# Performance work log

Measured on AMD Instinct MI355X. Metric: run time of the kernel, lower is better.

The kernel has to match this reference:

```python
import jax, jax.numpy as jnp
import numpy as np

B, S, D = 2, 2048, 4096
H, HKV, HD = 32, 8, 128          # heads, kv heads, head_dim
G = H // HKV                      # query groups per kv head
THETA = 10000.0


def setup_inputs() -> dict:
    key = jax.random.key(0)
    ks = jax.random.split(key, 6)
    s = 0.02
    return {
        "hidden_states": jax.random.normal(ks[0], (B, S, D), jnp.float32),
        "position_ids": jnp.broadcast_to(jnp.arange(S, dtype=jnp.int32), (B, S)),
        "attention_mask": jnp.ones((B, S), jnp.int32),
        "Wq": jax.random.normal(ks[1], (D, H * HD), jnp.float32) * s,
        "Wk": jax.random.normal(ks[2], (D, HKV * HD), jnp.float32) * s,
        "Wv": jax.random.normal(ks[3], (D, HKV * HD), jnp.float32) * s,
        "Wo": jax.random.normal(ks[4], (H * HD, D), jnp.float32) * s,
    }


def _rope_neox(x, positions):
    # x: [B, S, h, HD]; neox style: rotate halves
    half = HD // 2
    inv_freq = 1.0 / (THETA ** (jnp.arange(0, half, dtype=jnp.float32) / half))
    freqs = positions.astype(jnp.float32)[..., None] * inv_freq  # [B,S,half]
    cos = jnp.cos(freqs)[:, :, None, :]
    sin = jnp.sin(freqs)[:, :, None, :]
    x1, x2 = x[..., :half], x[..., half:]
    return jnp.concatenate([x1 * cos - x2 * sin, x2 * cos + x1 * sin], axis=-1)


def reference(hidden_states, position_ids, attention_mask, Wq, Wk, Wv, Wo):
    q = (hidden_states @ Wq).reshape(B, S, H, HD)
    k = (hidden_states @ Wk).reshape(B, S, HKV, HD)
    v = (hidden_states @ Wv).reshape(B, S, HKV, HD)

    q = _rope_neox(q, position_ids)
    k = _rope_neox(k, position_ids)

    # GQA: group query heads onto kv heads
    qg = q.reshape(B, S, HKV, G, HD)
    scale = HD ** -0.5
    scores = jnp.einsum("bqhgd,bkhd->bhgqk", qg, k) * scale  # [B,HKV,G,S,S]

    causal = jnp.tril(jnp.ones((S, S), bool))
    mask = causal[None, None, None] & (attention_mask[:, None, None, None, :] > 0)
    scores = jnp.where(mask, scores, jnp.finfo(scores.dtype).min)
    probs = jax.nn.softmax(scores, axis=-1)

    ctx = jnp.einsum("bhgqk,bkhd->bqhgd", probs, v).reshape(B, S, H * HD)
    return ctx @ Wo
```

## Files before the change

### kernel.cpp

```cpp
#include <hip/hip_runtime.h>
#include <hip/hip_bf16.h>
#include <cstdint>
#include <cstddef>

#define BB 2
#define SS 2048
#define DD 4096
#define HH 32
#define HKV 8
#define HDIM 128
#define NQKV 6144

typedef __attribute__((ext_vector_type(8))) short bf16x8;
typedef __attribute__((ext_vector_type(4))) float f32x4;

#define GLOAD_LDS16(g, l) __builtin_amdgcn_global_load_lds( \
    (const __attribute__((address_space(1))) void*)(g), \
    (__attribute__((address_space(3))) void*)(l), 16, 0, 0)

__global__ void cast_bf16_kernel(const float* __restrict__ in,
                                 __hip_bfloat16* __restrict__ out, int n4) {
  int i = blockIdx.x * 256 + threadIdx.x;
  if (i >= n4) return;
  float4 v = ((const float4*)in)[i];
  union { __hip_bfloat16 h[4]; short4 s4; } u;
  u.h[0] = __float2bfloat16(v.x);
  u.h[1] = __float2bfloat16(v.y);
  u.h[2] = __float2bfloat16(v.z);
  u.h[3] = __float2bfloat16(v.w);
  ((short4*)out)[i] = u.s4;
}

__global__ void transpose_cast4_kernel(const float* __restrict__ Wq,
                                       const float* __restrict__ Wk,
                                       const float* __restrict__ Wv,
                                       const float* __restrict__ Wo,
                                       __hip_bfloat16* __restrict__ WqkvT,
                                       __hip_bfloat16* __restrict__ WoT) {
  __shared__ float tile[32][33];
  int id = blockIdx.x;
  const float* W; __hip_bfloat16* WT; int C, bx, by;
  if (id < 16384)      { W = Wq; WT = WqkvT;                         C = 4096; int l = id;         bx = l & 127; by = l >> 7; }
  else if (id < 20480) { W = Wk; WT = WqkvT + (size_t)4096 * 4096;   C = 1024; int l = id - 16384; bx = l & 31;  by = l >> 5; }
  else if (id < 24576) { W = Wv; WT = WqkvT + (size_t)5120 * 4096;   C = 1024; int l = id - 20480; bx = l & 31;  by = l >> 5; }
  else                 { W = Wo; WT = WoT;                           C = 4096; int l = id - 24576; bx = l & 127; by = l >> 7; }
  const int R = 4096;
  int c0 = bx * 32, r0 = by * 32;
  int tx = threadIdx.x, ty = threadIdx.y;
#pragma unroll
  for (int i = 0; i < 32; i += 8)
    tile[ty + i][tx] = W[(size_t)(r0 + ty + i) * C + c0 + tx];
  __syncthreads();
#pragma unroll
  for (int i = 0; i < 32; i += 8)
    WT[(size_t)(c0 + ty + i) * R + r0 + tx] = __float2bfloat16(tile[tx][ty + i]);
}

__global__ void vt_kernel(const __hip_bfloat16* __restrict__ QKV,
                          __hip_bfloat16* __restrict__ VT) {
  __shared__ __hip_bfloat16 tile[32][33];
  int c0 = blockIdx.x * 32;
  int r0 = blockIdx.y * 32;
  int tx = threadIdx.x, ty = threadIdx.y;
#pragma unroll
  for (int i = 0; i < 32; i += 8)
    tile[ty + i][tx] = QKV[(size_t)(r0 + ty + i) * NQKV + 5120 + c0 + tx];
  __syncthreads();
#pragma unroll
  for (int i = 0; i < 32; i += 8) {
    int r = r0 + tx;
    int c = c0 + ty + i;
    VT[((size_t)(r >> 11) * 1024 + c) * SS + (r & 2047)] = tile[tx][ty + i];
  }
}

__global__ void rope_kernel(__hip_bfloat16* __restrict__ QKV,
                            const int* __restrict__ pos_ids) {
  int r = blockIdx.x;
  float fpos = (float)pos_ids[r];
  __hip_bfloat16* row = QKV + (size_t)r * NQKV;
  for (int p = threadIdx.x; p < 2560; p += 256) {
    int base, i;
    if (p < 2048) { base = (p >> 6) * HDIM; i = p & 63; }
    else { int q = p - 2048; base = DD + (q >> 6) * HDIM; i = q & 63; }
    float inv = exp2f(-(float)i * 0.20762050593046015f);
    float f = fpos * inv;
    float c = cosf(f), s = sinf(f);
    float x1 = __bfloat162float(row[base + i]);
    float x2 = __bfloat162float(row[base + i + 64]);
    row[base + i]      = __float2bfloat16(x1 * c - x2 * s);
    row[base + i + 64] = __float2bfloat16(x2 * c + x1 * s);
  }
}

template <int OUTF32>
__global__ __launch_bounds__(256) void gemm_bt_kernel(const __hip_bfloat16* __restrict__ A,
                                                      const __hip_bfloat16* __restrict__ BT,
                                                      void* __restrict__ Cout,
                                                      int M, int N, int K) {
  __shared__ alignas(16) __hip_bfloat16 As[128 * 32];
  __shared__ alignas(16) __hip_bfloat16 Bs[128 * 32];
  int bn = blockIdx.x, bm = blockIdx.y;
  int tid = threadIdx.x, wave = tid >> 6, lane = tid & 63;
  int lr = lane & 15, lq = lane >> 4;
  int wm = (wave >> 1) * 64, wn = (wave & 1) * 64;
  int row0 = bm * 128, col0 = bn * 128;
  int swz = lq ^ ((lr >> 1) & 3);
  f32x4 acc[4][4] = {};
  for (int k0 = 0; k0 < K; k0 += 32) {
    __syncthreads();
#pragma unroll
    for (int i = 0; i < 2; ++i) {
      int c = tid + i * 256;
      int r = c >> 2, cl = c & 3;
      int cg = cl ^ ((r >> 1) & 3);
      GLOAD_LDS16(A + (size_t)(row0 + r) * K + k0 + cg * 8, As + (size_t)c * 8);
      GLOAD_LDS16(BT + (size_t)(col0 + r) * K + k0 + cg * 8, Bs + (size_t)c * 8);
    }
    __syncthreads();
    bf16x8 af[4], bfb[4];
#pragma unroll
    for (int mt = 0; mt < 4; ++mt)
      af[mt] = *(const bf16x8*)(As + ((wm + mt * 16 + lr) * 4 + swz) * 8);
#pragma unroll
    for (int nt = 0; nt < 4; ++nt)
      bfb[nt] = *(const bf16x8*)(Bs + ((wn + nt * 16 + lr) * 4 + swz) * 8);
#pragma unroll
    for (int mt = 0; mt < 4; ++mt)
#pragma unroll
      for (int nt = 0; nt < 4; ++nt)
        acc[mt][nt] = __builtin_amdgcn_mfma_f32_16x16x32_bf16(af[mt], bfb[nt], acc[mt][nt], 0, 0, 0);
  }
#pragma unroll
  for (int mt = 0; mt < 4; ++mt)
#pragma unroll
    for (int nt = 0; nt < 4; ++nt)
#pragma unroll
      for (int r = 0; r < 4; ++r) {
        int row = row0 + wm + mt * 16 + lq * 4 + r;
        int col = col0 + wn + nt * 16 + lr;
        if (OUTF32) ((float*)Cout)[(size_t)row * N + col] = acc[mt][nt][r];
        else ((__hip_bfloat16*)Cout)[(size_t)row * N + col] = __float2bfloat16(acc[mt][nt][r]);
      }
}

#define PSTRIDE 72
__global__ __launch_bounds__(256) void attn_kernel(const __hip_bfloat16* __restrict__ QKV,
                                                   const __hip_bfloat16* __restrict__ VT,
                                                   __hip_bfloat16* __restrict__ Ctx) {
  __shared__ alignas(16) __hip_bfloat16 Ks[64 * 128];
  __shared__ alignas(16) __hip_bfloat16 Vs[128 * 64];
  __shared__ alignas(16) __hip_bfloat16 Ps[4][32 * PSTRIDE];
  int h = blockIdx.y, b = blockIdx.z;
  int hkv = h >> 2;
  int tid = threadIdx.x, wave = tid >> 6, lane = tid & 63;
  int lr = lane & 15, lq = lane >> 4;
  const __hip_bfloat16* Kbase = QKV + (size_t)b * SS * NQKV + DD + hkv * HDIM;
  const __hip_bfloat16* Vbase = VT + (size_t)(b * HKV + hkv) * HDIM * SS;
  const float scale = 0.08838834764831845f;

  for (int half = 0; half < 2; ++half) {
    int qt = half ? (15 - blockIdx.x) : blockIdx.x;
    int q0 = qt * 128 + wave * 32;

    bf16x8 qfrag[2][4];
#pragma unroll
    for (int mt = 0; mt < 2; ++mt) {
      const __hip_bfloat16* qrow = QKV + (size_t)(b * SS + q0 + mt * 16 + lr) * NQKV + h * HDIM;
#pragma unroll
      for (int ks = 0; ks < 4; ++ks) qfrag[mt][ks] = *(const bf16x8*)(qrow + ks * 32 + lq * 8);
    }

    f32x4 accO[2][8] = {};
    float m_r[2][4], l_r[2][4];
#pragma unroll
    for (int mt = 0; mt < 2; ++mt)
#pragma unroll
      for (int r = 0; r < 4; ++r) { m_r[mt][r] = -1e30f; l_r[mt][r] = 0.f; }

    int kv_end = qt * 128 + 128;
    for (int kv0 = 0; kv0 < kv_end; kv0 += 64) {
      __syncthreads();
#pragma unroll
      for (int i = 0; i < 4; ++i) {
        int c = tid + i * 256;
        int r = c >> 4, cl = c & 15, cg = cl ^ (r & 15);
        GLOAD_LDS16(Kbase + (size_t)(kv0 + r) * NQKV + cg * 8, Ks + (size_t)c * 8);
      }
#pragma unroll
      for (int i = 0; i < 4; ++i) {
        int c = tid + i * 256;
        int r = c >> 3, cl = c & 7, cg = cl ^ (r & 7);
        GLOAD_LDS16(Vbase + (size_t)r * SS + kv0 + cg * 8, Vs + (size_t)c * 8);
      }
      __syncthreads();

      f32x4 sc[2][4] = {};
#pragma unroll
      for (int nt = 0; nt < 4; ++nt)
#pragma unroll
        for (int ks = 0; ks < 4; ++ks) {
          int cl = (ks * 4 + lq) ^ lr;
          bf16x8 kf = *(const bf16x8*)(Ks + ((nt * 16 + lr) * 16 + cl) * 8);
#pragma unroll
          for (int mt = 0; mt < 2; ++mt)
            sc[mt][nt] = __builtin_amdgcn_mfma_f32_16x16x32_bf16(qfrag[mt][ks], kf, sc[mt][nt], 0, 0, 0);
        }

      if (kv0 + 64 > qt * 128) {
#pragma unroll
        for (int mt = 0; mt < 2; ++mt)
#pragma unroll
          for (int nt = 0; nt < 4; ++nt)
#pragma unroll
            for (int r = 0; r < 4; ++r) {
              float v = sc[mt][nt][r] * scale;
              int qp = q0 + mt * 16 + lq * 4 + r;
              int kp = kv0 + nt * 16 + lr;
              sc[mt][nt][r] = (kp > qp) ? -1e30f : v;
            }
      } else {
#pragma unroll
        for (int mt = 0; mt < 2; ++mt)
#pragma unroll
          for (int nt = 0; nt < 4; ++nt)
#pragma unroll
            for (int r = 0; r < 4; ++r) sc[mt][nt][r] *= scale;
      }

      float alpha[2][4];
#pragma unroll
      for (int mt = 0; mt < 2; ++mt)
#pragma unroll
        for (int r = 0; r < 4; ++r) {
          float mx = fmaxf(fmaxf(sc[mt][0][r], sc[mt][1][r]), fmaxf(sc[mt][2][r], sc[mt][3][r]));
#pragma unroll
          for (int d = 1; d < 16; d <<= 1) mx = fmaxf(mx, __shfl_xor(mx, d));
          float mnew = fmaxf(m_r[mt][r], mx);
          alpha[mt][r] = __expf(m_r[mt][r] - mnew);
          m_r[mt][r] = mnew;
        }
#pragma unroll
      for (int mt = 0; mt < 2; ++mt)
#pragma unroll
        for (int nt = 0; nt < 4; ++nt)
#pragma unroll
          for (int r = 0; r < 4; ++r) sc[mt][nt][r] = __expf(sc[mt][nt][r] - m_r[mt][r]);
#pragma unroll
      for (int mt = 0; mt < 2; ++mt)
#pragma unroll
        for (int r = 0; r < 4; ++r) {
          float sm = (sc[mt][0][r] + sc[mt][1][r]) + (sc[mt][2][r] + sc[mt][3][r]);
#pragma unroll
          for (int d = 1; d < 16; d <<= 1) sm += __shfl_xor(sm, d);
          l_r[mt][r] = l_r[mt][r] * alpha[mt][r] + sm;
        }
#pragma unroll
      for (int mt = 0; mt < 2; ++mt)
#pragma unroll
        for (int t = 0; t < 8; ++t)
#pragma unroll
          for (int r = 0; r < 4; ++r) accO[mt][t][r] *= alpha[mt][r];

      __hip_bfloat16* P = Ps[wave];
#pragma unroll
      for (int mt = 0; mt < 2; ++mt)
#pragma unroll
        for (int nt = 0; nt < 4; ++nt)
#pragma unroll
          for (int r = 0; r < 4; ++r)
            P[(mt * 16 + lq * 4 + r) * PSTRIDE + nt * 16 + lr] = __float2bfloat16(sc[mt][nt][r]);

#pragma unroll
      for (int ks2 = 0; ks2 < 2; ++ks2) {
        bf16x8 pf[2];
#pragma unroll
        for (int mt = 0; mt < 2; ++mt)
          pf[mt] = *(const bf16x8*)(P + (mt * 16 + lr) * PSTRIDE + ks2 * 32 + lq * 8);
#pragma unroll
        for (int t = 0; t < 8; ++t) {
          int cl = (ks2 * 4 + lq) ^ (lr & 7);
          bf16x8 vf = *(const bf16x8*)(Vs + ((t * 16 + lr) * 8 + cl) * 8);
#pragma unroll
          for (int mt = 0; mt < 2; ++mt)
            accO[mt][t] = __builtin_amdgcn_mfma_f32_16x16x32_bf16(pf[mt], vf, accO[mt][t], 0, 0, 0);
        }
      }
    }

#pragma unroll
    for (int mt = 0; mt < 2; ++mt)
#pragma unroll
      for (int t = 0; t < 8; ++t)
#pragma unroll
        for (int r = 0; r < 4; ++r) {
          float o = accO[mt][t][r] / l_r[mt][r];
          int row = q0 + mt * 16 + lq * 4 + r;
          int col = h * HDIM + t * 16 + lr;
          Ctx[(size_t)(b * SS + row) * (HH * HDIM) + col] = __float2bfloat16(o);
        }
  }
}

extern "C" void kernel_launch(void* const* d_in, const int* in_sizes, int n_in,
                              void* d_out, int out_size, void* d_ws, size_t ws_size,
                              hipStream_t stream) {
  const float* X  = (const float*)d_in[0];
  const int* pos  = (const int*)d_in[1];
  const float* Wq = (const float*)d_in[3];
  const float* Wk = (const float*)d_in[4];
  const float* Wv = (const float*)d_in[5];
  const float* Wo = (const float*)d_in[6];
  float* out = (float*)d_out;

  char* ws = (char*)d_ws;
  __hip_bfloat16* Xb    = (__hip_bfloat16*)(ws);
  __hip_bfloat16* Ctx   = (__hip_bfloat16*)(ws);
  __hip_bfloat16* WqkvT = (__hip_bfloat16*)(ws + 33554432);
  __hip_bfloat16* WoT   = (__hip_bfloat16*)(ws + 83886080);
  __hip_bfloat16* QKV   = (__hip_bfloat16*)(ws + 117440512);
  __hip_bfloat16* VT    = (__hip_bfloat16*)(ws + 167772160);

  const int n4 = (BB * SS * DD) / 4;
  cast_bf16_kernel<<<dim3(n4 / 256), dim3(256), 0, stream>>>(X, Xb, n4);

  transpose_cast4_kernel<<<dim3(40960), dim3(32, 8), 0, stream>>>(Wq, Wk, Wv, Wo, WqkvT, WoT);

  gemm_bt_kernel<0><<<dim3(6144 / 128, 4096 / 128), dim3(256), 0, stream>>>(Xb, WqkvT, QKV, 4096, 6144, 4096);

  rope_kernel<<<dim3(BB * SS), dim3(256), 0, stream>>>(QKV, pos);
  vt_kernel<<<dim3(1024 / 32, 4096 / 32), dim3(32, 8), 0, stream>>>(QKV, VT);

  attn_kernel<<<dim3(SS / 256, HH, BB), dim3(256), 0, stream>>>(QKV, VT, Ctx);

  gemm_bt_kernel<1><<<dim3(4096 / 128, 4096 / 128), dim3(256), 0, stream>>>(Ctx, WoT, out, 4096, 4096, 4096);
}
```

Before: 947.8 us.

## Use 32x32 MFMA with K=64 tiles in GEMM and restructure attention grid

```diff
diff --git a/kernel.cpp b/kernel.cpp
--- a/kernel.cpp
+++ b/kernel.cpp
@@ -13,6 +13,7 @@
 
 typedef __attribute__((ext_vector_type(8))) short bf16x8;
 typedef __attribute__((ext_vector_type(4))) float f32x4;
+typedef __attribute__((ext_vector_type(16))) float f32x16;
 
 #define GLOAD_LDS16(g, l) __builtin_amdgcn_global_load_lds( \
     (const __attribute__((address_space(1))) void*)(g), \
@@ -98,60 +99,67 @@
                                                       const __hip_bfloat16* __restrict__ BT,
                                                       void* __restrict__ Cout,
                                                       int M, int N, int K) {
-  __shared__ alignas(16) __hip_bfloat16 As[128 * 32];
-  __shared__ alignas(16) __hip_bfloat16 Bs[128 * 32];
+  __shared__ alignas(16) __hip_bfloat16 As[128 * 64];
+  __shared__ alignas(16) __hip_bfloat16 Bs[128 * 64];
   int bn = blockIdx.x, bm = blockIdx.y;
   int tid = threadIdx.x, wave = tid >> 6, lane = tid & 63;
-  int lr = lane & 15, lq = lane >> 4;
+  int lm = lane & 31, lh = lane >> 5;
   int wm = (wave >> 1) * 64, wn = (wave & 1) * 64;
   int row0 = bm * 128, col0 = bn * 128;
-  int swz = lq ^ ((lr >> 1) & 3);
-  f32x4 acc[4][4] = {};
-  for (int k0 = 0; k0 < K; k0 += 32) {
+  f32x16 acc[2][2] = {};
+  for (int k0 = 0; k0 < K; k0 += 64) {
     __syncthreads();
 #pragma unroll
-    for (int i = 0; i < 2; ++i) {
+    for (int i = 0; i < 4; ++i) {
       int c = tid + i * 256;
-      int r = c >> 2, cl = c & 3;
-      int cg = cl ^ ((r >> 1) & 3);
+      int r = c >> 3, cl = c & 7;
+      int cg = cl ^ (r & 7);
       GLOAD_LDS16(A + (size_t)(row0 + r) * K + k0 + cg * 8, As + (size_t)c * 8);
       GLOAD_LDS16(BT + (size_t)(col0 + r) * K + k0 + cg * 8, Bs + (size_t)c * 8);
     }
     __syncthreads();
-    bf16x8 af[4], bfb[4];
-#pragma unroll
-    for (int mt = 0; mt < 4; ++mt)
-      af[mt] = *(const bf16x8*)(As + ((wm + mt * 16 + lr) * 4 + swz) * 8);
-#pragma unroll
-    for (int nt = 0; nt < 4; ++nt)
-      bfb[nt] = *(const bf16x8*)(Bs + ((wn + nt * 16 + lr) * 4 + swz) * 8);
-#pragma unroll
-    for (int mt = 0; mt < 4; ++mt)
-#pragma unroll
-      for (int nt = 0; nt < 4; ++nt)
-        acc[mt][nt] = __builtin_amdgcn_mfma_f32_16x16x32_bf16(af[mt], bfb[nt], acc[mt][nt], 0, 0, 0);
-  }
-#pragma unroll
-  for (int mt = 0; mt < 4; ++mt)
-#pragma unroll
-    for (int nt = 0; nt < 4; ++nt)
-#pragma unroll
-      for (int r = 0; r < 4; ++r) {
-        int row = row0 + wm + mt * 16 + lq * 4 + r;
-        int col = col0 + wn + nt * 16 + lr;
+#pragma unroll
+    for (int ks = 0; ks < 4; ++ks) {
+      bf16x8 af[2], bfb[2];
+#pragma unroll
+      for (int mt = 0; mt < 2; ++mt) {
+        int cl = (ks * 2 + lh) ^ (lm & 7);
+        af[mt] = *(const bf16x8*)(As + (wm + mt * 32 + lm) * 64 + cl * 8);
+      }
+#pragma unroll
+      for (int nt = 0; nt < 2; ++nt) {
+        int cl = (ks * 2 + lh) ^ (lm & 7);
+        bfb[nt] = *(const bf16x8*)(Bs + (wn + nt * 32 + lm) * 64 + cl * 8);
+      }
+#pragma unroll
+      for (int mt = 0; mt < 2; ++mt)
+#pragma unroll
+        for (int nt = 0; nt < 2; ++nt)
+          acc[mt][nt] = __builtin_amdgcn_mfma_f32_32x32x16_bf16(af[mt], bfb[nt], acc[mt][nt], 0, 0, 0);
+    }
+  }
+#pragma unroll
+  for (int mt = 0; mt < 2; ++mt)
+#pragma unroll
+    for (int nt = 0; nt < 2; ++nt)
+#pragma unroll
+      for (int r = 0; r < 16; ++r) {
+        int row = row0 + wm + mt * 32 + (r & 3) + 8 * (r >> 2) + 4 * lh;
+        int col = col0 + wn + nt * 32 + lm;
         if (OUTF32) ((float*)Cout)[(size_t)row * N + col] = acc[mt][nt][r];
         else ((__hip_bfloat16*)Cout)[(size_t)row * N + col] = __float2bfloat16(acc[mt][nt][r]);
       }
 }
 
-#define PSTRIDE 72
 __global__ __launch_bounds__(256) void attn_kernel(const __hip_bfloat16* __restrict__ QKV,
                                                    const __hip_bfloat16* __restrict__ VT,
                                                    __hip_bfloat16* __restrict__ Ctx) {
   __shared__ alignas(16) __hip_bfloat16 Ks[64 * 128];
   __shared__ alignas(16) __hip_bfloat16 Vs[128 * 64];
-  __shared__ alignas(16) __hip_bfloat16 Ps[4][32 * PSTRIDE];
-  int h = blockIdx.y, b = blockIdx.z;
+  __shared__ alignas(16) __hip_bfloat16 Ps[4][32 * 64];
+  int hb = blockIdx.x;
+  int h = hb & 31, b = hb >> 5;
+  int qt = 15 - blockIdx.y;
   int hkv = h >> 2;
   int tid = threadIdx.x, wave = tid >> 6, lane = tid & 63;
   int lr = lane & 15, lq = lane >> 4;
@@ -159,147 +167,149 @@
   const __hip_bfloat16* Vbase = VT + (size_t)(b * HKV + hkv) * HDIM * SS;
   const float scale = 0.08838834764831845f;
 
-  for (int half = 0; half < 2; ++half) {
-    int qt = half ? (15 - blockIdx.x) : blockIdx.x;
-    int q0 = qt * 128 + wave * 32;
-
-    bf16x8 qfrag[2][4];
-#pragma unroll
-    for (int mt = 0; mt < 2; ++mt) {
-      const __hip_bfloat16* qrow = QKV + (size_t)(b * SS + q0 + mt * 16 + lr) * NQKV + h * HDIM;
-#pragma unroll
-      for (int ks = 0; ks < 4; ++ks) qfrag[mt][ks] = *(const bf16x8*)(qrow + ks * 32 + lq * 8);
-    }
-
-    f32x4 accO[2][8] = {};
-    float m_r[2][4], l_r[2][4];
-#pragma unroll
-    for (int mt = 0; mt < 2; ++mt)
-#pragma unroll
-      for (int r = 0; r < 4; ++r) { m_r[mt][r] = -1e30f; l_r[mt][r] = 0.f; }
-
-    int kv_end = qt * 128 + 128;
-    for (int kv0 = 0; kv0 < kv_end; kv0 += 64) {
-      __syncthreads();
-#pragma unroll
-      for (int i = 0; i < 4; ++i) {
-        int c = tid + i * 256;
-        int r = c >> 4, cl = c & 15, cg = cl ^ (r & 15);
-        GLOAD_LDS16(Kbase + (size_t)(kv0 + r) * NQKV + cg * 8, Ks + (size_t)c * 8);
-      }
-#pragma unroll
-      for (int i = 0; i < 4; ++i) {
-        int c = tid + i * 256;
-        int r = c >> 3, cl = c & 7, cg = cl ^ (r & 7);
-        GLOAD_LDS16(Vbase + (size_t)r * SS + kv0 + cg * 8, Vs + (size_t)c * 8);
-      }
-      __syncthreads();
-
-      f32x4 sc[2][4] = {};
+  int q0 = qt * 128 + wave * 32;
+
+  bf16x8 qfrag[2][4];
+#pragma unroll
+  for (int mt = 0; mt < 2; ++mt) {
+    const __hip_bfloat16* qrow = QKV + (size_t)(b * SS + q0 + mt * 16 + lr) * NQKV + h * HDIM;
+#pragma unroll
+    for (int ks = 0; ks < 4; ++ks) qfrag[mt][ks] = *(const bf16x8*)(qrow + ks * 32 + lq * 8);
+  }
+
+  f32x4 accO[2][8] = {};
+  float m_r[2][4], l_r[2][4];
+#pragma unroll
+  for (int mt = 0; mt < 2; ++mt)
+#pragma unroll
+    for (int r = 0; r < 4; ++r) { m_r[mt][r] = -1e30f; l_r[mt][r] = 0.f; }
+
+  int kv_end = qt * 128 + 128;
+  for (int kv0 = 0; kv0 < kv_end; kv0 += 64) {
+    __syncthreads();
+#pragma unroll
+    for (int i = 0; i < 4; ++i) {
+      int c = tid + i * 256;
+      int r = c >> 4, cl = c & 15, cg = cl ^ (r & 15);
+      GLOAD_LDS16(Kbase + (size_t)(kv0 + r) * NQKV + cg * 8, Ks + (size_t)c * 8);
+    }
+#pragma unroll
+    for (int i = 0; i < 4; ++i) {
+      int c = tid + i * 256;
+      int r = c >> 3, cl = c & 7, cg = cl ^ (r & 7);
+      GLOAD_LDS16(Vbase + (size_t)r * SS + kv0 + cg * 8, Vs + (size_t)c * 8);
+    }
+    __syncthreads();
+
+    f32x4 sc[2][4] = {};
+#pragma unroll
+    for (int nt = 0; nt < 4; ++nt)
+#pragma unroll
+      for (int ks = 0; ks < 4; ++ks) {
+        int cl = (ks * 4 + lq) ^ lr;
+        bf16x8 kf = *(const bf16x8*)(Ks + ((nt * 16 + lr) * 16 + cl) * 8);
+#pragma unroll
+        for (int mt = 0; mt < 2; ++mt)
+          sc[mt][nt] = __builtin_amdgcn_mfma_f32_16x16x32_bf16(qfrag[mt][ks], kf, sc[mt][nt], 0, 0, 0);
+      }
+
+    if (kv0 + 64 > qt * 128) {
+#pragma unroll
+      for (int mt = 0; mt < 2; ++mt)
+#pragma unroll
+        for (int nt = 0; nt < 4; ++nt)
+#pragma unroll
+          for (int r = 0; r < 4; ++r) {
+            float v = sc[mt][nt][r] * scale;
+            int qp = q0 + mt * 16 + lq * 4 + r;
+            int kp = kv0 + nt * 16 + lr;
+            sc[mt][nt][r] = (kp > qp) ? -1e30f : v;
+          }
+    } else {
+#pragma unroll
+      for (int mt = 0; mt < 2; ++mt)
+#pragma unroll
+        for (int nt = 0; nt < 4; ++nt)
+#pragma unroll
+          for (int r = 0; r < 4; ++r) sc[mt][nt][r] *= scale;
+    }
+
+    float alpha[2][4];
+#pragma unroll
+    for (int mt = 0; mt < 2; ++mt)
+#pragma unroll
+      for (int r = 0; r < 4; ++r) {
+        float mx = fmaxf(fmaxf(sc[mt][0][r], sc[mt][1][r]), fmaxf(sc[mt][2][r], sc[mt][3][r]));
+#pragma unroll
+        for (int d = 1; d < 16; d <<= 1) mx = fmaxf(mx, __shfl_xor(mx, d));
+        float mnew = fmaxf(m_r[mt][r], mx);
+        alpha[mt][r] = __expf(m_r[mt][r] - mnew);
+        m_r[mt][r] = mnew;
+      }
+#pragma unroll
+    for (int mt = 0; mt < 2; ++mt)
 #pragma unroll
       for (int nt = 0; nt < 4; ++nt)
 #pragma unroll
-        for (int ks = 0; ks < 4; ++ks) {
-          int cl = (ks * 4 + lq) ^ lr;
-          bf16x8 kf = *(const bf16x8*)(Ks + ((nt * 16 + lr) * 16 + cl) * 8);
-#pragma unroll
-          for (int mt = 0; mt < 2; ++mt)
-            sc[mt][nt] = __builtin_amdgcn_mfma_f32_16x16x32_bf16(qfrag[mt][ks], kf, sc[mt][nt], 0, 0, 0);
+        for (int r = 0; r < 4; ++r) sc[mt][nt][r] = __expf(sc[mt][nt][r] - m_r[mt][r]);
+#pragma unroll
+    for (int mt = 0; mt < 2; ++mt)
+#pragma unroll
+      for (int r = 0; r < 4; ++r) {
+        float sm = (sc[mt][0][r] + sc[mt][1][r]) + (sc[mt][2][r] + sc[mt][3][r]);
+#pragma unroll
+        for (int d = 1; d < 16; d <<= 1) sm += __shfl_xor(sm, d);
+        l_r[mt][r] = l_r[mt][r] * alpha[mt][r] + sm;
+      }
+#pragma unroll
+    for (int mt = 0; mt < 2; ++mt)
+#pragma unroll
+      for (int t = 0; t < 8; ++t)
+#pragma unroll
+        for (int r = 0; r < 4; ++r) accO[mt][t][r] *= alpha[mt][r];
+
+    __hip_bfloat16* P = Ps[wave];
+#pragma unroll
+    for (int mt = 0; mt < 2; ++mt)
+#pragma unroll
+      for (int nt = 0; nt < 4; ++nt)
+#pragma unroll
+        for (int r = 0; r < 4; ++r) {
+          int row = mt * 16 + lq * 4 + r;
+          int cs = (nt * 2 + (lr >> 3)) ^ (row & 7);
+          P[row * 64 + cs * 8 + (lr & 7)] = __float2bfloat16(sc[mt][nt][r]);
         }
 
-      if (kv0 + 64 > qt * 128) {
+#pragma unroll
+    for (int ks2 = 0; ks2 < 2; ++ks2) {
+      bf16x8 pf[2];
+#pragma unroll
+      for (int mt = 0; mt < 2; ++mt) {
+        int row = mt * 16 + lr;
+        pf[mt] = *(const bf16x8*)(P + row * 64 + (((ks2 * 4 + lq) ^ (row & 7))) * 8);
+      }
+#pragma unroll
+      for (int t = 0; t < 8; ++t) {
+        int cl = (ks2 * 4 + lq) ^ (lr & 7);
+        bf16x8 vf = *(const bf16x8*)(Vs + ((t * 16 + lr) * 8 + cl) * 8);
 #pragma unroll
         for (int mt = 0; mt < 2; ++mt)
-#pragma unroll
-          for (int nt = 0; nt < 4; ++nt)
-#pragma unroll
-            for (int r = 0; r < 4; ++r) {
-              float v = sc[mt][nt][r] * scale;
-              int qp = q0 + mt * 16 + lq * 4 + r;
-              int kp = kv0 + nt * 16 + lr;
-              sc[mt][nt][r] = (kp > qp) ? -1e30f : v;
-            }
-      } else {
-#pragma unroll
-        for (int mt = 0; mt < 2; ++mt)
-#pragma unroll
-          for (int nt = 0; nt < 4; ++nt)
-#pragma unroll
-            for (int r = 0; r < 4; ++r) sc[mt][nt][r] *= scale;
-      }
-
-      float alpha[2][4];
-#pragma unroll
-      for (int mt = 0; mt < 2; ++mt)
-#pragma unroll
-        for (int r = 0; r < 4; ++r) {
-          float mx = fmaxf(fmaxf(sc[mt][0][r], sc[mt][1][r]), fmaxf(sc[mt][2][r], sc[mt][3][r]));
-#pragma unroll
-          for (int d = 1; d < 16; d <<= 1) mx = fmaxf(mx, __shfl_xor(mx, d));
-          float mnew = fmaxf(m_r[mt][r], mx);
-          alpha[mt][r] = __expf(m_r[mt][r] - mnew);
-          m_r[mt][r] = mnew;
-        }
-#pragma unroll
-      for (int mt = 0; mt < 2; ++mt)
-#pragma unroll
-        for (int nt = 0; nt < 4; ++nt)
-#pragma unroll
-          for (int r = 0; r < 4; ++r) sc[mt][nt][r] = __expf(sc[mt][nt][r] - m_r[mt][r]);
-#pragma unroll
-      for (int mt = 0; mt < 2; ++mt)
-#pragma unroll
-        for (int r = 0; r < 4; ++r) {
-          float sm = (sc[mt][0][r] + sc[mt][1][r]) + (sc[mt][2][r] + sc[mt][3][r]);
-#pragma unroll
-          for (int d = 1; d < 16; d <<= 1) sm += __shfl_xor(sm, d);
-          l_r[mt][r] = l_r[mt][r] * alpha[mt][r] + sm;
-        }
-#pragma unroll
-      for (int mt = 0; mt < 2; ++mt)
-#pragma unroll
-        for (int t = 0; t < 8; ++t)
-#pragma unroll
-          for (int r = 0; r < 4; ++r) accO[mt][t][r] *= alpha[mt][r];
-
-      __hip_bfloat16* P = Ps[wave];
-#pragma unroll
-      for (int mt = 0; mt < 2; ++mt)
-#pragma unroll
-        for (int nt = 0; nt < 4; ++nt)
-#pragma unroll
-          for (int r = 0; r < 4; ++r)
-            P[(mt * 16 + lq * 4 + r) * PSTRIDE + nt * 16 + lr] = __float2bfloat16(sc[mt][nt][r]);
-
-#pragma unroll
-      for (int ks2 = 0; ks2 < 2; ++ks2) {
-        bf16x8 pf[2];
-#pragma unroll
-        for (int mt = 0; mt < 2; ++mt)
-          pf[mt] = *(const bf16x8*)(P + (mt * 16 + lr) * PSTRIDE + ks2 * 32 + lq * 8);
-#pragma unroll
-        for (int t = 0; t < 8; ++t) {
-          int cl = (ks2 * 4 + lq) ^ (lr & 7);
-          bf16x8 vf = *(const bf16x8*)(Vs + ((t * 16 + lr) * 8 + cl) * 8);
-#pragma unroll
-          for (int mt = 0; mt < 2; ++mt)
-            accO[mt][t] = __builtin_amdgcn_mfma_f32_16x16x32_bf16(pf[mt], vf, accO[mt][t], 0, 0, 0);
-        }
-      }
-    }
-
-#pragma unroll
-    for (int mt = 0; mt < 2; ++mt)
-#pragma unroll
-      for (int t = 0; t < 8; ++t)
-#pragma unroll
-        for (int r = 0; r < 4; ++r) {
-          float o = accO[mt][t][r] / l_r[mt][r];
-          int row = q0 + mt * 16 + lq * 4 + r;
-          int col = h * HDIM + t * 16 + lr;
-          Ctx[(size_t)(b * SS + row) * (HH * HDIM) + col] = __float2bfloat16(o);
-        }
-  }
+          accO[mt][t] = __builtin_amdgcn_mfma_f32_16x16x32_bf16(pf[mt], vf, accO[mt][t], 0, 0, 0);
+      }
+    }
+  }
+
+#pragma unroll
+  for (int mt = 0; mt < 2; ++mt)
+#pragma unroll
+    for (int t = 0; t < 8; ++t)
+#pragma unroll
+      for (int r = 0; r < 4; ++r) {
+        float o = accO[mt][t][r] / l_r[mt][r];
+        int row = q0 + mt * 16 + lq * 4 + r;
+        int col = h * HDIM + t * 16 + lr;
+        Ctx[(size_t)(b * SS + row) * (HH * HDIM) + col] = __float2bfloat16(o);
+      }
 }
 
 extern "C" void kernel_launch(void* const* d_in, const int* in_sizes, int n_in,
@@ -331,7 +341,7 @@
   rope_kernel<<<dim3(BB * SS), dim3(256), 0, stream>>>(QKV, pos);
   vt_kernel<<<dim3(1024 / 32, 4096 / 32), dim3(32, 8), 0, stream>>>(QKV, VT);
 
-  attn_kernel<<<dim3(SS / 256, HH, BB), dim3(256), 0, stream>>>(QKV, VT, Ctx);
+  attn_kernel<<<dim3(64, 16), dim3(256), 0, stream>>>(QKV, VT, Ctx);
 
   gemm_bt_kernel<1><<<dim3(4096 / 128, 4096 / 128), dim3(256), 0, stream>>>(Ctx, WoT, out, 4096, 4096, 4096);
 }
```

Measured after the change: 858.0 us. -9.5%, faster.
